# Kernel tuning notes

Hardware: AMD Instinct MI355X
Metric: run time of the kernel (lower is better)

Reference implementation:

```python
import jax, jax.numpy as jnp
import numpy as np
from jax import lax

HID = 2048; NK = 16; NV = 32; DK = 128; DV = 128; KSZ = 4; CHUNK = 64; S = 2048
KEY_DIM = NK * DK; VAL_DIM = NV * DV; CONV_DIM = 2 * KEY_DIM + VAL_DIM
EPS = 1e-6


def l2norm(x, eps=1e-6):
    return x * lax.rsqrt((x * x).sum(-1, keepdims=True) + eps)


def chunk_gated_delta_rule(q, k, v, g, beta, chunk=CHUNK):
    # q,k: [B,S,Hv,DK]; v: [B,S,Hv,DV]; g,beta: [B,S,Hv]
    q = l2norm(q); k = l2norm(k)  # use_qk_l2norm_in_kernel=True
    q, k, v = (jnp.swapaxes(x, 1, 2) for x in (q, k, v))  # [B,H,S,D]
    g = jnp.swapaxes(g, 1, 2); beta = jnp.swapaxes(beta, 1, 2)  # [B,H,S]
    B, H, Ssz, Dk = k.shape; Dv = v.shape[-1]
    N = Ssz // chunk  # seq_len chosen divisible by chunk -> pad is no-op
    q = q * (Dk ** -0.5)
    vb = v * beta[..., None]
    kb = k * beta[..., None]
    rs = lambda x: x.reshape(B, H, N, chunk, x.shape[-1])
    q, k, v, kb, vb = map(rs, (q, k, v, kb, vb))
    g = jnp.cumsum(g.reshape(B, H, N, chunk), axis=-1)
    tril = jnp.tril(jnp.ones((chunk, chunk), bool))
    stril = jnp.tril(jnp.ones((chunk, chunk), bool), -1)
    diff = jnp.where(tril, g[..., :, None] - g[..., None, :], 0.0)
    decay_mask = jnp.where(tril, jnp.exp(diff), 0.0)  # [B,H,N,C,C]
    attn = jnp.where(stril, -(kb @ jnp.swapaxes(k, -1, -2)) * decay_mask, 0.0)
    # UT (WY) transform: sequential row updates, scan over in-chunk index
    def ut_body(a, i):
        row = jnp.take(a, i, axis=-2)  # [B,H,N,C]
        new = row + jnp.einsum('bhnk,bhnkj->bhnj', row, a)
        return a.at[:, :, :, i, :].set(new), None
    attn, _ = lax.scan(ut_body, attn, jnp.arange(1, chunk))
    attn = attn + jnp.eye(chunk, dtype=attn.dtype)
    u = attn @ vb                                   # [B,H,N,C,DV]
    kcd = attn @ (kb * jnp.exp(g)[..., None])       # [B,H,N,C,DK]
    init = jnp.zeros((B, H, Dk, Dv), q.dtype)
    def step(state, inp):
        q_i, k_i, u_i, kcd_i, g_i, dm_i = inp
        scores = (q_i @ jnp.swapaxes(k_i, -1, -2)) * dm_i
        v_new = u_i - kcd_i @ state
        inter = (q_i * jnp.exp(g_i)[..., None]) @ state
        o = inter + scores @ v_new
        gl = g_i[..., -1]  # [B,H]
        state = state * jnp.exp(gl)[..., None, None] + jnp.einsum(
            'bhcd,bhce->bhde', k_i * jnp.exp(gl[..., None] - g_i)[..., None], v_new)
        return state, o
    mv = lambda x: jnp.moveaxis(x, 2, 0)
    _, out = lax.scan(step, init, (mv(q), mv(k), mv(u), mv(kcd), mv(g), mv(decay_mask)))
    out = jnp.moveaxis(out, 0, 2).reshape(B, H, Ssz, Dv)
    return jnp.swapaxes(out, 1, 2)  # [B,S,H,DV]


def setup_inputs() -> dict:
    key = jax.random.key(0)
    ks = jax.random.split(key, 8)
    return {
        'hidden_states': jax.random.normal(ks[0], (S, HID), jnp.float32),
        'W_qkv': jax.random.normal(ks[1], (CONV_DIM, HID), jnp.float32) * 0.02,
        'W_z': jax.random.normal(ks[2], (VAL_DIM, HID), jnp.float32) * 0.02,
        'W_a': jax.random.normal(ks[3], (NV, HID), jnp.float32) * 0.02,
        'W_b': jax.random.normal(ks[4], (NV, HID), jnp.float32) * 0.02,
        'conv_w': jax.random.normal(ks[5], (CONV_DIM, 1, KSZ), jnp.float32) * 0.1,
        'dt_bias': jnp.ones((NV,), jnp.float32),
        'A_log': jnp.log(jax.random.uniform(ks[6], (NV,), jnp.float32, 0.1, 16.0)),
        'norm_w': jnp.ones((DV,), jnp.float32),
        'W_out': jax.random.normal(ks[7], (HID, VAL_DIM), jnp.float32) * 0.02,
    }


def reference(hidden_states, W_qkv, W_z, W_a, W_b, conv_w, dt_bias, A_log, norm_w, W_out):
    x = hidden_states  # [S, HID]
    mixed = x @ W_qkv.T  # [S, CONV_DIM]
    z = (x @ W_z.T).reshape(-1, DV)  # [S*NV, DV]
    a = x @ W_a.T  # [S, NV]
    b = x @ W_b.T
    # causal depthwise conv1d (torch pads K-1 both sides then slices [:S])
    conv = lax.conv_general_dilated(
        mixed.T[None], conv_w, (1,), [(KSZ - 1, 0)],
        dimension_numbers=('NCH', 'OIH', 'NCH'), feature_group_count=CONV_DIM)
    mixed = jax.nn.silu(conv[0].T)  # [S, CONV_DIM]
    q = mixed[:, :KEY_DIM].reshape(1, S, NK, DK)
    k = mixed[:, KEY_DIM:2 * KEY_DIM].reshape(1, S, NK, DK)
    v = mixed[:, 2 * KEY_DIM:].reshape(1, S, NV, DV)
    beta = jax.nn.sigmoid(b)[None]  # [1,S,NV]
    g = (-jnp.exp(A_log) * jax.nn.softplus(a + dt_bias))[None]  # [1,S,NV]
    ratio = NV // NK
    q = jnp.repeat(q, ratio, axis=2)
    k = jnp.repeat(k, ratio, axis=2)
    core = chunk_gated_delta_rule(q, k, v, g, beta)  # [1,S,NV,DV]
    h = core.reshape(-1, DV)  # [S*NV, DV]
    var = jnp.mean(h * h, axis=-1, keepdims=True)
    h = h * lax.rsqrt(var + EPS) * norm_w
    h = h * jax.nn.silu(z)
    out = h.reshape(S, VAL_DIM) @ W_out.T  # [S, HID]
    return out
```

## Files before the change

### kernel.cpp

```cpp
#include <hip/hip_runtime.h>
#include <hip/hip_bf16.h>
#include <math.h>

#define S_LEN   2048
#define HIDDIM  2048
#define NKH     16
#define NVH     32
#define DKD     128
#define DVD     128
#define CCH     64
#define NCHK    32
#define KEY_DIM 2048
#define VAL_DIM 4096
#define CONV_DIM 8192

#define PA_LDS_BYTES (16384 + 16384 + 32768 + 4096 + 4096 + 256 + 256 + 256)
#define PB_LDS_BYTES ((2 * 29696 + 2048 + 1024 + 1024) * 2 + 2048 * 4)
#define G256_LDS_BYTES (3 * 16384 * 2)
#define G128_LDS_BYTES (3 * 8192 * 2)

typedef __bf16 bf16x8 __attribute__((ext_vector_type(8)));
typedef float f32x4 __attribute__((ext_vector_type(4)));

__device__ __forceinline__ float sigmoid_f(float x) { return 1.f / (1.f + __expf(-x)); }
__device__ __forceinline__ float silu_f(float x) { return x * sigmoid_f(x); }
__device__ __forceinline__ ushort f2bf(float f) {
    unsigned u = __float_as_uint(f);
    u += 0x7fffu + ((u >> 16) & 1u);
    return (ushort)(u >> 16);
}
__device__ __forceinline__ float bf2f(ushort u) {
    return __uint_as_float((unsigned)u << 16);
}

#define GLL(srcp, dstp) __builtin_amdgcn_global_load_lds( \
    (const __attribute__((address_space(1))) void*)(srcp), \
    (__attribute__((address_space(3))) void*)(dstp), 16, 0, 0)

#define NX8  (S_LEN * HIDDIM / 8)
#define NQ8  (CONV_DIM * HIDDIM / 8)
#define NZ8  (VAL_DIM * HIDDIM / 8)
#define NW8  (HIDDIM * VAL_DIM / 8)
#define NA8  (256 * HIDDIM / 8)
__global__ __launch_bounds__(256) void cast5_kernel(
    const float* __restrict__ x, const float* __restrict__ Wq,
    const float* __restrict__ Wz, const float* __restrict__ Wo,
    const float* __restrict__ Wa, const float* __restrict__ Wb,
    ushort* __restrict__ xb, ushort* __restrict__ wqz, ushort* __restrict__ wob,
    ushort* __restrict__ wab)
{
    int t = blockIdx.x * 256 + threadIdx.x;
    const float* src;
    ushort* dst;
    if (t < NX8) { src = x + (size_t)t * 8; dst = xb + (size_t)t * 8; }
    else if (t < NX8 + NQ8) {
        size_t o = (size_t)(t - NX8) * 8;
        src = Wq + o; dst = wqz + o;
    } else if (t < NX8 + NQ8 + NZ8) {
        size_t o = (size_t)(t - NX8 - NQ8) * 8;
        src = Wz + o; dst = wqz + (size_t)NQ8 * 8 + o;
    } else if (t < NX8 + NQ8 + NZ8 + NW8) {
        size_t o = (size_t)(t - NX8 - NQ8 - NZ8) * 8;
        src = Wo + o; dst = wob + o;
    } else {
        int g = t - NX8 - NQ8 - NZ8 - NW8;
        int row = g >> 8;
        int c8 = (g & 255) * 8;
        dst = wab + (size_t)g * 8;
        if (row >= 64) {
            uint4 z = {0, 0, 0, 0};
            *(uint4*)dst = z;
            return;
        }
        src = (row < 32) ? (Wa + (size_t)row * HIDDIM + c8)
                         : (Wb + (size_t)(row - 32) * HIDDIM + c8);
    }
    float4 v0 = *(const float4*)(src);
    float4 v1 = *(const float4*)(src + 4);
    union { ushort u[8]; uint4 v; } r;
    r.u[0] = f2bf(v0.x); r.u[1] = f2bf(v0.y); r.u[2] = f2bf(v0.z); r.u[3] = f2bf(v0.w);
    r.u[4] = f2bf(v1.x); r.u[5] = f2bf(v1.y); r.u[6] = f2bf(v1.z); r.u[7] = f2bf(v1.w);
    *(uint4*)dst = r.v;
}

__global__ __launch_bounds__(512, 1) void gemm256_kernel(
    const ushort* __restrict__ A, const ushort* __restrict__ B,
    ushort* __restrict__ C0, ushort* __restrict__ C1, float* __restrict__ C2,
    int K, int NS1, int NS2, int ldc0, int ldc1, int ldc2)
{
    extern __shared__ ushort g2s[];
    const int tid = threadIdx.x;
    const int wv = tid >> 6, ln = tid & 63;
    const int wm = wv >> 1, wn = wv & 1;
    const int lrow = ln & 15, lkg = ln >> 4;
    const int bid = blockIdx.y * 49 + blockIdx.x;
    const int swz = (bid & 7) * 49 + (bid >> 3);
    const int bm = (swz / 49) * 256, bn = (swz % 49) * 256;

    int soff[2];
#pragma unroll
    for (int j = 0; j < 2; ++j) {
        int g = tid + j * 512;
        int l = g & 63;
        soff[j] = (((g >> 6) * 16) + (l & 15)) * K + (l >> 4) * 8;
    }
    const ushort* Abase = A + (size_t)bm * K;
    const ushort* Bbase = B + (size_t)bn * K;

    f32x4 acc[4][8];
#pragma unroll
    for (int m = 0; m < 4; ++m)
#pragma unroll
        for (int n = 0; n < 8; ++n) {
            f32x4 z = {0.f, 0.f, 0.f, 0.f};
            acc[m][n] = z;
        }

#define G256_STAGE(bb, k0) do {                                            \
        ushort* bufA_ = g2s + (bb) * 16384;                                \
        ushort* bufB_ = bufA_ + 8192;                                      \
        _Pragma("unroll")                                                  \
        for (int j_ = 0; j_ < 2; ++j_) {                                   \
            GLL(Abase + soff[j_] + (k0), bufA_ + (j_ * 512 + wv * 64) * 8);\
            GLL(Bbase + soff[j_] + (k0), bufB_ + (j_ * 512 + wv * 64) * 8);\
        }                                                                  \
    } while (0)

    const int T = K >> 5;
    G256_STAGE(0, 0);
    G256_STAGE(1, 32);
    int bb = 0;
    for (int t = 0; t < T; ++t) {
        if (t + 1 < T) {
            asm volatile("s_waitcnt vmcnt(4)" ::: "memory");
        } else {
            asm volatile("s_waitcnt vmcnt(0)" ::: "memory");
        }
        __builtin_amdgcn_s_barrier();
        if (t + 2 < T) G256_STAGE((bb >= 1) ? (bb - 1) : (bb + 2), (t + 2) * 32);
        const ushort* LA = g2s + bb * 16384;
        const ushort* LB = LA + 8192;
        __builtin_amdgcn_s_setprio(1);
        {
            bf16x8 afv[4], bfv[8];
#pragma unroll
            for (int mf = 0; mf < 4; ++mf)
                afv[mf] = *(const bf16x8*)&LA[((wm * 4 + mf) * 64 + ln) * 8];
#pragma unroll
            for (int nf = 0; nf < 8; ++nf)
                bfv[nf] = *(const bf16x8*)&LB[((wn * 8 + nf) * 64 + ln) * 8];
#pragma unroll
            for (int mf = 0; mf < 4; ++mf)
#pragma unroll
                for (int nf = 0; nf < 8; ++nf)
                    acc[mf][nf] = __builtin_amdgcn_mfma_f32_16x16x32_bf16(
                        afv[mf], bfv[nf], acc[mf][nf], 0, 0, 0);
        }
        __builtin_amdgcn_s_setprio(0);
        bb = (bb == 2) ? 0 : bb + 1;
    }
#undef G256_STAGE

    if (bn < NS2) {
        const bool inC1 = (bn >= NS1);
        ushort* Cp = inC1 ? C1 : C0;
        const int ldc = inC1 ? ldc1 : ldc0;
        const int cboff = bn + wn * 128 - (inC1 ? NS1 : 0);
#pragma unroll
        for (int mf = 0; mf < 4; ++mf) {
            const int row0 = bm + wm * 64 + mf * 16 + lkg * 4;
#pragma unroll
            for (int nf = 0; nf < 8; ++nf) {
                ushort* cp = Cp + (size_t)row0 * ldc + cboff + nf * 16 + lrow;
#pragma unroll
                for (int j = 0; j < 4; ++j) cp[(size_t)j * ldc] = f2bf(acc[mf][nf][j]);
            }
        }
    } else {
        const int cboff = bn + wn * 128 - NS2;
#pragma unroll
        for (int mf = 0; mf < 4; ++mf) {
            const int row0 = bm + wm * 64 + mf * 16 + lkg * 4;
#pragma unroll
            for (int nf = 0; nf < 8; ++nf) {
                float* cp = C2 + (size_t)row0 * ldc2 + cboff + nf * 16 + lrow;
#pragma unroll
                for (int j = 0; j < 4; ++j) cp[(size_t)j * ldc2] = acc[mf][nf][j];
            }
        }
    }
}

__global__ __launch_bounds__(256, 2) void gemm128_kernel(
    const ushort* __restrict__ A, const ushort* __restrict__ B,
    float* __restrict__ C, int N, int K)
{
    extern __shared__ ushort g1s[];
    const int tid = threadIdx.x;
    const int wv = tid >> 6, ln = tid & 63;
    const int wm = wv >> 1, wn = wv & 1;
    const int lrow = ln & 15, lkg = ln >> 4;
    const int bm = blockIdx.y * 128, bn = blockIdx.x * 128;

    int soff[2];
#pragma unroll
    for (int j = 0; j < 2; ++j) {
        int g = tid + j * 256;
        int l = g & 63;
        soff[j] = (((g >> 6) * 16) + (l & 15)) * K + (l >> 4) * 8;
    }
    const ushort* Abase = A + (size_t)bm * K;
    const ushort* Bbase = B + (size_t)bn * K;

    f32x4 acc[4][4];
#pragma unroll
    for (int m = 0; m < 4; ++m)
#pragma unroll
        for (int n = 0; n < 4; ++n) {
            f32x4 z = {0.f, 0.f, 0.f, 0.f};
            acc[m][n] = z;
        }

#define G128_STAGE(bb, k0) do {                                            \
        ushort* bufA_ = g1s + (bb) * 8192;                                 \
        ushort* bufB_ = bufA_ + 4096;                                      \
        _Pragma("unroll")                                                  \
        for (int j_ = 0; j_ < 2; ++j_) {                                   \
            GLL(Abase + soff[j_] + (k0), bufA_ + (j_ * 256 + wv * 64) * 8);\
            GLL(Bbase + soff[j_] + (k0), bufB_ + (j_ * 256 + wv * 64) * 8);\
        }                                                                  \
    } while (0)

    const int T = K >> 5;
    G128_STAGE(0, 0);
    G128_STAGE(1, 32);
    int bb = 0;
    for (int t = 0; t < T; ++t) {
        if (t + 1 < T) {
            asm volatile("s_waitcnt vmcnt(4)" ::: "memory");
        } else {
            asm volatile("s_waitcnt vmcnt(0)" ::: "memory");
        }
        __builtin_amdgcn_s_barrier();
        if (t + 2 < T) G128_STAGE((bb >= 1) ? (bb - 1) : (bb + 2), (t + 2) * 32);
        const ushort* LA = g1s + bb * 8192;
        const ushort* LB = LA + 4096;
        __builtin_amdgcn_s_setprio(1);
        {
            bf16x8 afv[4], bfv[4];
#pragma unroll
            for (int mf = 0; mf < 4; ++mf)
                afv[mf] = *(const bf16x8*)&LA[((wm * 4 + mf) * 64 + ln) * 8];
#pragma unroll
            for (int nf = 0; nf < 4; ++nf)
                bfv[nf] = *(const bf16x8*)&LB[((wn * 4 + nf) * 64 + ln) * 8];
#pragma unroll
            for (int mf = 0; mf < 4; ++mf)
#pragma unroll
                for (int nf = 0; nf < 4; ++nf)
                    acc[mf][nf] = __builtin_amdgcn_mfma_f32_16x16x32_bf16(
                        afv[mf], bfv[nf], acc[mf][nf], 0, 0, 0);
        }
        __builtin_amdgcn_s_setprio(0);
        bb = (bb == 2) ? 0 : bb + 1;
    }
#undef G128_STAGE

#pragma unroll
    for (int mf = 0; mf < 4; ++mf) {
        const int row0 = bm + wm * 64 + mf * 16 + lkg * 4;
#pragma unroll
        for (int nf = 0; nf < 4; ++nf) {
            float* cp = C + (size_t)row0 * N + bn + wn * 64 + nf * 16 + lrow;
#pragma unroll
            for (int j = 0; j < 4; ++j) cp[(size_t)j * N] = acc[mf][nf][j];
        }
    }
}

__global__ __launch_bounds__(256) void front_kernel(
    const ushort* __restrict__ pre, const float* __restrict__ cw,
    ushort* __restrict__ qnb, ushort* __restrict__ knb, ushort* __restrict__ vbuf)
{
    __shared__ float stage[4096];
    __shared__ float sums[32];
    __shared__ float scal[32];
    const int s = blockIdx.x;
    const int tid = threadIdx.x;

#pragma unroll
    for (int cg = 0; cg < 8; ++cg) {
        const int c = cg * 1024 + tid * 4;
        float w[4][4];
#pragma unroll
        for (int j = 0; j < 4; ++j) {
            float4 wj = *(const float4*)(cw + (size_t)(c + j) * 4);
            w[j][0] = wj.x; w[j][1] = wj.y; w[j][2] = wj.z; w[j][3] = wj.w;
        }
        float a0 = 0.f, a1 = 0.f, a2 = 0.f, a3 = 0.f;
#pragma unroll
        for (int t = 0; t < 4; ++t) {
            int ss = s - 3 + t;
            if (ss >= 0) {
                uint2 xv = *(const uint2*)(pre + (size_t)ss * CONV_DIM + c);
                a0 = fmaf(bf2f((ushort)xv.x), w[0][t], a0);
                a1 = fmaf(bf2f((ushort)(xv.x >> 16)), w[1][t], a1);
                a2 = fmaf(bf2f((ushort)xv.y), w[2][t], a2);
                a3 = fmaf(bf2f((ushort)(xv.y >> 16)), w[3][t], a3);
            }
        }
        a0 = silu_f(a0); a1 = silu_f(a1); a2 = silu_f(a2); a3 = silu_f(a3);
        if (cg < 4) {
            float4 v4 = make_float4(a0, a1, a2, a3);
            *(float4*)&stage[c] = v4;
            float ss2 = a0 * a0 + a1 * a1 + a2 * a2 + a3 * a3;
#pragma unroll
            for (int m = 1; m < 32; m <<= 1) ss2 += __shfl_xor(ss2, m, 32);
            if ((tid & 31) == 0) sums[c >> 7] = ss2;
        } else {
            union { ushort u2[4]; uint2 v; } p;
            p.u2[0] = f2bf(a0); p.u2[1] = f2bf(a1);
            p.u2[2] = f2bf(a2); p.u2[3] = f2bf(a3);
            *(uint2*)(vbuf + (size_t)s * VAL_DIM + (c - 4096)) = p.v;
        }
    }
    __syncthreads();
    if (tid < 32) {
        float sc = rsqrtf(sums[tid] + 1e-6f);
        if (tid < 16) sc *= 0.08838834764831843f;
        scal[tid] = sc;
    }
    __syncthreads();
#pragma unroll
    for (int j = 0; j < 4; ++j) {
        const int c = j * 1024 + tid * 4;
        float4 v4 = *(const float4*)&stage[c];
        const float sc = scal[c >> 7];
        union { ushort u2[4]; uint2 v; } p;
        p.u2[0] = f2bf(v4.x * sc); p.u2[1] = f2bf(v4.y * sc);
        p.u2[2] = f2bf(v4.z * sc); p.u2[3] = f2bf(v4.w * sc);
        if (c < 2048)
            *(uint2*)(qnb + ((size_t)(s * NKH + (c >> 7))) * DKD + (c & 127)) = p.v;
        else
            *(uint2*)(knb + ((size_t)(s * NKH + ((c >> 7) - 16))) * DKD + (c & 127)) = p.v;
    }
}

__global__ __launch_bounds__(256) void gb_kernel(
    const float* __restrict__ ab, const float* __restrict__ dt_bias,
    const float* __restrict__ A_log, float* __restrict__ g, float* __restrict__ beta)
{
    int idx = blockIdx.x * 256 + threadIdx.x;
    int s = idx >> 5, h = idx & 31;
    float av = ab[(size_t)s * 256 + h] + dt_bias[h];
    float sp = (av > 20.f) ? av : log1pf(__expf(av));
    g[idx] = -__expf(A_log[h]) * sp;
    beta[idx] = sigmoid_f(ab[(size_t)s * 256 + 32 + h]);
}

__global__ __launch_bounds__(256) void phaseA_kernel(
    const ushort* __restrict__ qnb, const ushort* __restrict__ knb,
    const ushort* __restrict__ vbuf, const float* __restrict__ gbuf,
    const float* __restrict__ betabuf,
    ushort* __restrict__ u, ushort* __restrict__ kcd,
    ushort* __restrict__ scores, float* __restrict__ gcs_out,
    ushort* __restrict__ knT)
{
    extern __shared__ char pasm[];
    ushort* kb    = (ushort*)(pasm);
    ushort* qb    = (ushort*)(pasm + 16384);
    ushort* Xb    = (ushort*)(pasm + 32768);
    float*  Adiag = (float*)(pasm + 65536);
    ushort* Ab    = (ushort*)(pasm + 69632);
    float*  gcs_s = (float*)(pasm + 73728);
    float*  bet_s = (float*)(pasm + 73984);
    float*  scK_s = (float*)(pasm + 74240);
    float*  Pf    = (float*)qb;

    const int n = blockIdx.x, h = blockIdx.y, kh = h >> 1;
    const int tid = threadIdx.x;
    const int s0 = n * CCH;
    const int wv = tid >> 6, ln = tid & 63;
    const int lrow = ln & 15, lkg = ln >> 4;

    float xr[64];
    if (tid < 128) {
        const ushort* vp = vbuf + (size_t)s0 * VAL_DIM + h * DVD + tid;
#pragma unroll
        for (int i = 0; i < 64; ++i) xr[i] = bf2f(vp[(size_t)i * VAL_DIM]);
    } else {
        const ushort* kp = knb + ((size_t)s0 * NKH + kh) * DKD + (tid - 128);
#pragma unroll
        for (int i = 0; i < 64; ++i) xr[i] = bf2f(kp[(size_t)i * (NKH * DKD)]);
    }

    {
        uint4 z = {0, 0, 0, 0};
#pragma unroll
        for (int i = 0; i < 8; ++i)
            *(uint4*)&Xb[(i * 256 + tid) * 8] = z;
        *(uint4*)&Ab[tid * 8] = z;
    }

    if (tid < 64) {
        float gv = gbuf[(size_t)(s0 + tid) * NVH + h];
#pragma unroll
        for (int off = 1; off < 64; off <<= 1) {
            float pv = __shfl_up(gv, off, 64);
            if (tid >= off) gv += pv;
        }
        float bv = betabuf[(size_t)(s0 + tid) * NVH + h];
        gcs_s[tid] = gv;
        bet_s[tid] = bv;
        scK_s[tid] = bv * __expf(gv);
        gcs_out[(size_t)h * S_LEN + s0 + tid] = gv;
    }

    {
        const int r = tid >> 2, c0 = (tid & 3) * 32;
        const int mbase = (((r >> 4) * 4 + (tid & 3)) * 64 + (r & 15)) * 8;
        const ushort* ksrc = knb + ((size_t)(s0 + r) * NKH + kh) * DKD + c0;
        const ushort* qsrc = qnb + ((size_t)(s0 + r) * NKH + kh) * DKD + c0;
#pragma unroll
        for (int j0 = 0; j0 < 4; ++j0) {
            *(uint4*)&kb[mbase + (j0 << 7)] = *(const uint4*)(ksrc + j0 * 8);
            *(uint4*)&qb[mbase + (j0 << 7)] = *(const uint4*)(qsrc + j0 * 8);
        }
    }
    __syncthreads();

    f32x4 accA[4], accQ[4];
#pragma unroll
    for (int j = 0; j < 4; ++j) {
        f32x4 z = {0.f, 0.f, 0.f, 0.f};
        accA[j] = z; accQ[j] = z;
    }
#pragma unroll
    for (int ks = 0; ks < 4; ++ks) {
        bf16x8 a_k = *(const bf16x8*)&kb[((wv * 4 + ks) * 64 + ln) * 8];
        bf16x8 a_q = *(const bf16x8*)&qb[((wv * 4 + ks) * 64 + ln) * 8];
#pragma unroll
        for (int j = 0; j < 4; ++j) {
            bf16x8 b_k = *(const bf16x8*)&kb[((j * 4 + ks) * 64 + ln) * 8];
            accA[j] = __builtin_amdgcn_mfma_f32_16x16x32_bf16(a_k, b_k, accA[j], 0, 0, 0);
            accQ[j] = __builtin_amdgcn_mfma_f32_16x16x32_bf16(a_q, b_k, accQ[j], 0, 0, 0);
        }
    }
    {
        ushort* scp = scores + (size_t)(h * NCHK + n) * (CCH * CCH);
#pragma unroll
        for (int j = 0; j < 4; ++j) {
            const int c = j * 16 + lrow;
            const float gc = gcs_s[c];
#pragma unroll
            for (int jj = 0; jj < 4; ++jj) {
                const int i = wv * 16 + lkg * 4 + jj;
                const float e = __expf(gcs_s[i] - gc);
                float sv = (i >= c) ? (accQ[j][jj] * e) : 0.f;
                scp[i * CCH + c] = f2bf(sv);
                float aval = (i > c) ? (-bet_s[i] * accA[j][jj] * e) : 0.f;
                if (j == wv) {
                    Adiag[wv * 256 + (i & 15) * 16 + lrow] = aval;
                } else if (j < wv) {
                    const int f = (wv == 1) ? 0 : ((wv == 2) ? 1 : (2 + (j >> 1)));
                    const int lk = ((j & 1) << 4) | lrow;
                    const int lane2 = (i & 15) | ((lk >> 3) << 4);
                    Ab[(f * 64 + lane2) * 8 + (lk & 7)] = f2bf(aval);
                }
            }
        }
    }
    if (tid < 128) {
#pragma unroll
        for (int i4 = 0; i4 < 16; ++i4) {
            float4 b4 = *(const float4*)&bet_s[i4 * 4];
            xr[i4 * 4 + 0] *= b4.x; xr[i4 * 4 + 1] *= b4.y;
            xr[i4 * 4 + 2] *= b4.z; xr[i4 * 4 + 3] *= b4.w;
        }
    } else {
#pragma unroll
        for (int i4 = 0; i4 < 16; ++i4) {
            float4 b4 = *(const float4*)&scK_s[i4 * 4];
            xr[i4 * 4 + 0] *= b4.x; xr[i4 * 4 + 1] *= b4.y;
            xr[i4 * 4 + 2] *= b4.z; xr[i4 * 4 + 3] *= b4.w;
        }
    }
    __syncthreads();

    const int ct = tid >> 4, lct = tid & 15;
#pragma unroll
    for (int s = 0; s < 4; ++s) {
        float y[16];
        float pr[16];
        if (s > 0) {
#pragma unroll
            for (int r = 0; r < 16; ++r) pr[r] = Pf[r * 256 + tid];
        } else {
#pragma unroll
            for (int r = 0; r < 16; ++r) pr[r] = 0.f;
        }
#pragma unroll
        for (int r = 0; r < 16; ++r) {
            float acc = xr[s * 16 + r] + pr[r];
#pragma unroll
            for (int k4 = 0; k4 < 16; k4 += 4) {
                if (k4 < r) {
                    float4 a4 = *(const float4*)&Adiag[s * 256 + r * 16 + k4];
                    if (k4 + 0 < r) acc = fmaf(a4.x, y[k4 + 0], acc);
                    if (k4 + 1 < r) acc = fmaf(a4.y, y[k4 + 1], acc);
                    if (k4 + 2 < r) acc = fmaf(a4.z, y[k4 + 2], acc);
                    if (k4 + 3 < r) acc = fmaf(a4.w, y[k4 + 3], acc);
                }
            }
            y[r] = acc;
        }
        if (tid < 128) {
            ushort* up = u + (size_t)(h * NCHK + n) * (CCH * DVD) + (s * 16) * DVD + tid;
#pragma unroll
            for (int r = 0; r < 16; ++r) up[r * DVD] = f2bf(y[r]);
        } else {
            ushort* kp = kcd + (size_t)(h * NCHK + n) * (CCH * DKD) + (s * 16) * DKD + (tid - 128);
#pragma unroll
            for (int r = 0; r < 16; ++r) kp[r * DKD] = f2bf(y[r]);
        }
        if (s < 3) {
#pragma unroll
            for (int half = 0; half < 2; ++half) {
                union { ushort us[8]; uint4 v; } p;
#pragma unroll
                for (int e = 0; e < 8; ++e) p.us[e] = f2bf(y[half * 8 + e]);
                const int kg = (s & 1) * 2 + half;
                *(uint4*)&Xb[(((s >> 1) * 16 + ct) * 64 + (kg * 16 + lct)) * 8] = p.v;
            }
            __syncthreads();
            const int snx = s + 1;
            const int nT2 = (snx + 1) >> 1;
            f32x4 accP[4];
#pragma unroll
            for (int ctl = 0; ctl < 4; ++ctl) {
                f32x4 z = {0.f, 0.f, 0.f, 0.f};
                accP[ctl] = z;
            }
#pragma unroll
            for (int t2 = 0; t2 < 2; ++t2) {
                if (t2 < nT2) {
                    const int f = (snx == 1) ? 0 : ((snx == 2) ? 1 : (2 + t2));
                    bf16x8 a = *(const bf16x8*)&Ab[(f * 64 + ln) * 8];
#pragma unroll
                    for (int ctl = 0; ctl < 4; ++ctl) {
                        bf16x8 b = *(const bf16x8*)&Xb[((t2 * 16 + wv * 4 + ctl) * 64 + ln) * 8];
                        accP[ctl] = __builtin_amdgcn_mfma_f32_16x16x32_bf16(a, b, accP[ctl], 0, 0, 0);
                    }
                }
            }
#pragma unroll
            for (int ctl = 0; ctl < 4; ++ctl)
#pragma unroll
                for (int jj = 0; jj < 4; ++jj)
                    Pf[(lkg * 4 + jj) * 256 + wv * 64 + ctl * 16 + lrow] = accP[ctl][jj];
            __syncthreads();
        }
    }

    if (!(h & 1)) {
        const int dk = tid >> 1, ch = (tid & 1) * 32;
        ushort* dst = knT + ((size_t)(kh * NCHK + n) * DKD + dk) * CCH + ch;
        const int kpart = ((dk >> 5) * 64) * 8 + (((dk >> 3) & 3) << 4) * 8 + (dk & 7);
#pragma unroll
        for (int j0 = 0; j0 < 32; j0 += 8) {
            union { ushort us[8]; uint4 v; } p;
#pragma unroll
            for (int j = 0; j < 8; ++j) {
                const int row = ch + j0 + j;
                p.us[j] = kb[((row >> 4) * 4 * 64 + (row & 15)) * 8 + kpart];
            }
            *(uint4*)(dst + j0) = p.v;
        }
    }
}

__global__ __launch_bounds__(256) void phaseB_kernel(
    const ushort* __restrict__ qnb, const ushort* __restrict__ knT,
    const ushort* __restrict__ u, const ushort* __restrict__ kcd,
    const ushort* __restrict__ sc, const float* __restrict__ gcs,
    ushort* __restrict__ obuf)
{
    extern __shared__ ushort smu[];
    ushort* storg  = smu + 59392;
    ushort* vnorg  = smu + 61440;
    ushort* vnsorg = smu + 62464;
    float*  gcsall = (float*)(smu + 63488);

    const int h = blockIdx.x;
    const int dvb = blockIdx.y;
    const int d0 = dvb * 16;
    const int kh = h >> 1;
    const int tid = threadIdx.x;
    const int wv = tid >> 6, ln = tid & 63;
    const int lrow = ln & 15, lkg = ln >> 4;

    {
        uint4 z = {0, 0, 0, 0};
        *(uint4*)&storg[tid * 8] = z;
    }

    const int q_lane  = lrow * (NKH * DKD) + kh * DKD + wv * 32 + lkg * 8;
    const int kc_lane = lrow * DKD + wv * 32 + lkg * 8;
    const int st_lane = ((tid >> 7) * 16 + lrow) * 64 + ((tid >> 6) & 1) * 32 + lkg * 8;
    const int dst_e   = wv * 512;

#define PBSTG(bsel, nn) do {                                                  \
        const ushort* qsrc_  = qnb + (size_t)((nn) * CCH) * (NKH * DKD);      \
        const ushort* kcsrc_ = kcd + (size_t)(h * NCHK + (nn)) * (CCH * DKD); \
        const ushort* scsrc_ = sc  + (size_t)(h * NCHK + (nn)) * (CCH * CCH); \
        const ushort* kTsrc_ = knT + (size_t)(kh * NCHK + (nn)) * (DKD * CCH);\
        const ushort* usrc_  = u   + (size_t)(h * NCHK + (nn)) * (CCH * DVD) + d0; \
        ushort* base_ = smu + (bsel) * 29696;                                 \
        _Pragma("unroll")                                                     \
        for (int r_ = 0; r_ < 4; ++r_) {                                      \
            GLL(qsrc_ + q_lane + r_ * 32768, base_ + r_ * 2048 + dst_e);      \
            GLL(kcsrc_ + kc_lane + r_ * 2048, base_ + 8192 + r_ * 2048 + dst_e); \
            GLL(kTsrc_ + st_lane + r_ * 2048, base_ + 20480 + r_ * 2048 + dst_e); \
        }                                                                     \
        _Pragma("unroll")                                                     \
        for (int r_ = 0; r_ < 2; ++r_)                                        \
            GLL(scsrc_ + st_lane + r_ * 2048, base_ + 16384 + r_ * 2048 + dst_e); \
        if (tid < 128)                                                        \
            GLL(usrc_ + (tid >> 1) * DVD + (tid & 1) * 8, base_ + 28672 + tid * 8); \
    } while (0)

    PBSTG(0, 0);
    {
        float4 g0 = *(const float4*)(gcs + (size_t)h * S_LEN + tid * 8);
        float4 g1 = *(const float4*)(gcs + (size_t)h * S_LEN + tid * 8 + 4);
        *(float4*)&gcsall[tid * 8] = g0;
        *(float4*)&gcsall[tid * 8 + 4] = g1;
    }
    __syncthreads();

    f32x4 accS0 = {0.f, 0.f, 0.f, 0.f}, accS1 = {0.f, 0.f, 0.f, 0.f};

    for (int n = 0; n < NCHK; ++n) {
        const int cur = n & 1;
        if (n + 1 < NCHK) PBSTG(cur ^ 1, n + 1);
        const ushort* qorg  = smu + cur * 29696;
        const ushort* kcorg = qorg + 8192;
        const ushort* scorg = qorg + 16384;
        const ushort* kTorg = qorg + 20480;
        const ushort* uorg  = qorg + 28672;
        const float*  gcs_s = gcsall + n * 64;
        const int s0 = n * CCH;

        f32x4 accv = {0.f, 0.f, 0.f, 0.f};
        f32x4 acco = {0.f, 0.f, 0.f, 0.f};
#pragma unroll
        for (int ks = 0; ks < 4; ++ks) {
            bf16x8 b_st = *(const bf16x8*)&storg[(ks * 64 + ln) * 8];
            bf16x8 a_kc = *(const bf16x8*)&kcorg[((wv * 4 + ks) * 64 + ln) * 8];
            bf16x8 a_q  = *(const bf16x8*)&qorg[((wv * 4 + ks) * 64 + ln) * 8];
            accv = __builtin_amdgcn_mfma_f32_16x16x32_bf16(a_kc, b_st, accv, 0, 0, 0);
            acco = __builtin_amdgcn_mfma_f32_16x16x32_bf16(a_q, b_st, acco, 0, 0, 0);
        }
        const int row = wv * 16 + lkg * 4;
        float u0 = bf2f(uorg[(row + 0) * 16 + lrow]);
        float u1 = bf2f(uorg[(row + 1) * 16 + lrow]);
        float u2 = bf2f(uorg[(row + 2) * 16 + lrow]);
        float u3 = bf2f(uorg[(row + 3) * 16 + lrow]);
        const float gl = gcs_s[63];
        float vn0 = u0 - accv[0], vn1 = u1 - accv[1];
        float vn2 = u2 - accv[2], vn3 = u3 - accv[3];
        {
            float g0 = gcs_s[row], g1 = gcs_s[row + 1], g2 = gcs_s[row + 2], g3 = gcs_s[row + 3];
            acco[0] *= __expf(g0); acco[1] *= __expf(g1);
            acco[2] *= __expf(g2); acco[3] *= __expf(g3);
            const int eb = ((wv >> 1) * 64 + ((wv & 1) * 2 + (lkg >> 1)) * 16 + lrow) * 8
                         + (lkg & 1) * 4;
            union { ushort u2a[4]; uint2 v; } pa, pb;
            pa.u2a[0] = f2bf(vn0); pa.u2a[1] = f2bf(vn1);
            pa.u2a[2] = f2bf(vn2); pa.u2a[3] = f2bf(vn3);
            pb.u2a[0] = f2bf(vn0 * __expf(gl - g0)); pb.u2a[1] = f2bf(vn1 * __expf(gl - g1));
            pb.u2a[2] = f2bf(vn2 * __expf(gl - g2)); pb.u2a[3] = f2bf(vn3 * __expf(gl - g3));
            *(uint2*)&vnorg[eb] = pa.v;
            *(uint2*)&vnsorg[eb] = pb.v;
        }
        __syncthreads();

#pragma unroll
        for (int ks = 0; ks < 2; ++ks) {
            bf16x8 a_sc = *(const bf16x8*)&scorg[((wv * 2 + ks) * 64 + ln) * 8];
            bf16x8 b_vn = *(const bf16x8*)&vnorg[(ks * 64 + ln) * 8];
            acco = __builtin_amdgcn_mfma_f32_16x16x32_bf16(a_sc, b_vn, acco, 0, 0, 0);
        }
        ushort* op = obuf + (size_t)(s0 + row) * VAL_DIM + h * DVD + d0 + lrow;
        op[0] = f2bf(acco[0]); op[VAL_DIM] = f2bf(acco[1]);
        op[2 * VAL_DIM] = f2bf(acco[2]); op[3 * VAL_DIM] = f2bf(acco[3]);

        const float egl = __expf(gl);
        accS0 *= egl; accS1 *= egl;
#pragma unroll
        for (int ks = 0; ks < 2; ++ks) {
            bf16x8 a_vs = *(const bf16x8*)&vnsorg[(ks * 64 + ln) * 8];
            bf16x8 b_k0 = *(const bf16x8*)&kTorg[(((wv * 2 + 0) * 2 + ks) * 64 + ln) * 8];
            bf16x8 b_k1 = *(const bf16x8*)&kTorg[(((wv * 2 + 1) * 2 + ks) * 64 + ln) * 8];
            accS0 = __builtin_amdgcn_mfma_f32_16x16x32_bf16(a_vs, b_k0, accS0, 0, 0, 0);
            accS1 = __builtin_amdgcn_mfma_f32_16x16x32_bf16(a_vs, b_k1, accS1, 0, 0, 0);
        }
#pragma unroll
        for (int j = 0; j < 4; ++j) {
            storg[(wv * 64 + ((lrow >> 3)) * 16 + lkg * 4 + j) * 8 + (lrow & 7)] = f2bf(accS0[j]);
            storg[(wv * 64 + (2 + (lrow >> 3)) * 16 + lkg * 4 + j) * 8 + (lrow & 7)] = f2bf(accS1[j]);
        }
        __syncthreads();
    }
#undef PBSTG
}

__global__ __launch_bounds__(256) void norm_kernel(
    const ushort* __restrict__ obuf, const ushort* __restrict__ z,
    const float* __restrict__ nw, ushort* __restrict__ hbuf)
{
    int row = (blockIdx.x * 256 + threadIdx.x) >> 6;
    int lane = threadIdx.x & 63;
    uint ov = *(const uint*)(obuf + (size_t)row * DVD + lane * 2);
    float x0 = bf2f((ushort)ov), x1 = bf2f((ushort)(ov >> 16));
    float ss = x0 * x0 + x1 * x1;
#pragma unroll
    for (int m = 1; m < 64; m <<= 1) ss += __shfl_xor(ss, m, 64);
    float scale = rsqrtf(ss * (1.f / DVD) + 1e-6f);
    uint zv = *(const uint*)(z + (size_t)row * DVD + lane * 2);
    float z0 = bf2f((ushort)zv), z1 = bf2f((ushort)(zv >> 16));
    float2 w2 = *(const float2*)(nw + lane * 2);
    float h0 = x0 * scale * w2.x * silu_f(z0);
    float h1 = x1 * scale * w2.y * silu_f(z1);
    union { ushort u[2]; uint v; } r;
    r.u[0] = f2bf(h0); r.u[1] = f2bf(h1);
    *(uint*)(hbuf + (size_t)row * DVD + lane * 2) = r.v;
}

extern "C" void kernel_launch(void* const* d_in, const int* in_sizes, int n_in,
                              void* d_out, int out_size, void* d_ws, size_t ws_size,
                              hipStream_t stream)
{
    (void)in_sizes; (void)n_in; (void)out_size; (void)ws_size;
    const float* x      = (const float*)d_in[0];
    const float* W_qkv  = (const float*)d_in[1];
    const float* W_z    = (const float*)d_in[2];
    const float* W_a    = (const float*)d_in[3];
    const float* W_b    = (const float*)d_in[4];
    const float* conv_w = (const float*)d_in[5];
    const float* dt_b   = (const float*)d_in[6];
    const float* A_log  = (const float*)d_in[7];
    const float* norm_w = (const float*)d_in[8];
    const float* W_out  = (const float*)d_in[9];
    float* out = (float*)d_out;

    char* ws = (char*)d_ws;
    ushort* mixed_pre = (ushort*)(ws);
    ushort* u_buf     = (ushort*)(ws);
    ushort* kcd_buf   = (ushort*)(ws + 33554432);
    ushort* knT_buf   = (ushort*)(ws + 50331648);
    ushort* wqz       = (ushort*)(ws + 67108864);
    ushort* wab       = (ushort*)(ws + 117440512);
    ushort* xb        = (ushort*)(ws + 118489088);
    ushort* vbuf      = (ushort*)(ws + 67108864);
    ushort* obuf      = (ushort*)(ws + 83886080);
    ushort* hbuf      = (ushort*)(ws + 100663296);
    ushort* z_buf     = (ushort*)(ws + 134217728);
    ushort* sc_buf    = (ushort*)(ws + 167772160);
    float*  ab_buf    = (float*)(ws + 167772160);
    ushort* qnb       = (ushort*)(ws + 176160768);
    ushort* knb       = (ushort*)(ws + 184549376);
    float*  g_buf     = (float*)(ws + 201326592);
    float*  bet_buf   = (float*)(ws + 201588736);
    float*  gcs_buf   = (float*)(ws + 201850880);
    ushort* wob       = (ushort*)(ws + 202113024);

    hipFuncSetAttribute((const void*)phaseA_kernel,
                        hipFuncAttributeMaxDynamicSharedMemorySize, PA_LDS_BYTES);
    hipFuncSetAttribute((const void*)phaseB_kernel,
                        hipFuncAttributeMaxDynamicSharedMemorySize, PB_LDS_BYTES);
    hipFuncSetAttribute((const void*)gemm256_kernel,
                        hipFuncAttributeMaxDynamicSharedMemorySize, G256_LDS_BYTES);
    hipFuncSetAttribute((const void*)gemm128_kernel,
                        hipFuncAttributeMaxDynamicSharedMemorySize, G128_LDS_BYTES);

    dim3 blk(256);
    cast5_kernel<<<(NX8 + NQ8 + NZ8 + NW8 + NA8) / 256, blk, 0, stream>>>(
        x, W_qkv, W_z, W_out, W_a, W_b, xb, wqz, wob, wab);
    gemm256_kernel<<<dim3(49, S_LEN / 256), dim3(512), G256_LDS_BYTES, stream>>>(
        xb, wqz, mixed_pre, z_buf, ab_buf, HIDDIM,
        CONV_DIM, CONV_DIM + VAL_DIM, CONV_DIM, VAL_DIM, 256);
    front_kernel<<<S_LEN, blk, 0, stream>>>(mixed_pre, conv_w, qnb, knb, vbuf);
    gb_kernel<<<(S_LEN * NVH) / 256, blk, 0, stream>>>(ab_buf, dt_b, A_log, g_buf, bet_buf);
    phaseA_kernel<<<dim3(NCHK, NVH), blk, PA_LDS_BYTES, stream>>>(
        qnb, knb, vbuf, g_buf, bet_buf, u_buf, kcd_buf, sc_buf, gcs_buf, knT_buf);
    phaseB_kernel<<<dim3(NVH, 8), blk, PB_LDS_BYTES, stream>>>(
        qnb, knT_buf, u_buf, kcd_buf, sc_buf, gcs_buf, obuf);
    norm_kernel<<<(S_LEN * NVH * 64) / 256, blk, 0, stream>>>(obuf, z_buf, norm_w, hbuf);
    gemm128_kernel<<<dim3(HIDDIM / 128, S_LEN / 128), blk, G128_LDS_BYTES, stream>>>(
        hbuf, wob, out, HIDDIM, VAL_DIM);
}
```

Measured before the change: 408.5 us.

## Load GEMM A operand directly to registers and fuse gate computation into phaseA

In the large input-projection GEMM, the A tile is no longer staged through LDS. Each lane reads its A fragments straight from global memory into registers, which halves the LDS footprint and cuts the async copies per stage. The loop now issues its fragment loads before prefetching the next stage and places the barrier after the MFMAs. Separately, the small g/beta kernel is removed and its softplus/sigmoid math moves into phaseA's prologue, which saves a launch and an intermediate buffer. The risk is that uncached, strided direct global loads of A may stall the MFMA pipeline more than LDS staging did.

```diff
diff --git a/kernel.cpp b/kernel.cpp
--- a/kernel.cpp
+++ b/kernel.cpp
@@ -16,7 +16,7 @@
 
 #define PA_LDS_BYTES (16384 + 16384 + 32768 + 4096 + 4096 + 256 + 256 + 256)
 #define PB_LDS_BYTES ((2 * 29696 + 2048 + 1024 + 1024) * 2 + 2048 * 4)
-#define G256_LDS_BYTES (3 * 16384 * 2)
+#define G256_LDS_BYTES (3 * 8192 * 2)
 #define G128_LDS_BYTES (3 * 8192 * 2)
 
 typedef __bf16 bf16x8 __attribute__((ext_vector_type(8)));
@@ -104,8 +104,8 @@
         int l = g & 63;
         soff[j] = (((g >> 6) * 16) + (l & 15)) * K + (l >> 4) * 8;
     }
-    const ushort* Abase = A + (size_t)bm * K;
     const ushort* Bbase = B + (size_t)bn * K;
+    const ushort* Alane = A + (size_t)(bm + wm * 64 + lrow) * K + lkg * 8;
 
     f32x4 acc[4][8];
 #pragma unroll
@@ -117,46 +117,43 @@
         }
 
 #define G256_STAGE(bb, k0) do {                                            \
-        ushort* bufA_ = g2s + (bb) * 16384;                                \
-        ushort* bufB_ = bufA_ + 8192;                                      \
+        ushort* bufB_ = g2s + (bb) * 8192;                                 \
         _Pragma("unroll")                                                  \
-        for (int j_ = 0; j_ < 2; ++j_) {                                   \
-            GLL(Abase + soff[j_] + (k0), bufA_ + (j_ * 512 + wv * 64) * 8);\
+        for (int j_ = 0; j_ < 2; ++j_)                                     \
             GLL(Bbase + soff[j_] + (k0), bufB_ + (j_ * 512 + wv * 64) * 8);\
-        }                                                                  \
     } while (0)
 
     const int T = K >> 5;
     G256_STAGE(0, 0);
     G256_STAGE(1, 32);
+    asm volatile("s_waitcnt vmcnt(2)" ::: "memory");
+    __builtin_amdgcn_s_barrier();
     int bb = 0;
     for (int t = 0; t < T; ++t) {
-        if (t + 1 < T) {
-            asm volatile("s_waitcnt vmcnt(4)" ::: "memory");
+        const ushort* LB = g2s + bb * 8192;
+        bf16x8 bfv[8];
+#pragma unroll
+        for (int nf = 0; nf < 8; ++nf)
+            bfv[nf] = *(const bf16x8*)&LB[((wn * 8 + nf) * 64 + ln) * 8];
+        bf16x8 afv[4];
+#pragma unroll
+        for (int mf = 0; mf < 4; ++mf)
+            afv[mf] = *(const bf16x8*)(Alane + (size_t)(mf * 16) * K + t * 32);
+        if (t + 2 < T) G256_STAGE((bb >= 1) ? (bb - 1) : (bb + 2), (t + 2) * 32);
+        if (t + 2 < T) {
+            asm volatile("s_waitcnt vmcnt(2)" ::: "memory");
         } else {
             asm volatile("s_waitcnt vmcnt(0)" ::: "memory");
         }
+        __builtin_amdgcn_s_setprio(1);
+#pragma unroll
+        for (int mf = 0; mf < 4; ++mf)
+#pragma unroll
+            for (int nf = 0; nf < 8; ++nf)
+                acc[mf][nf] = __builtin_amdgcn_mfma_f32_16x16x32_bf16(
+                    afv[mf], bfv[nf], acc[mf][nf], 0, 0, 0);
+        __builtin_amdgcn_s_setprio(0);
         __builtin_amdgcn_s_barrier();
-        if (t + 2 < T) G256_STAGE((bb >= 1) ? (bb - 1) : (bb + 2), (t + 2) * 32);
-        const ushort* LA = g2s + bb * 16384;
-        const ushort* LB = LA + 8192;
-        __builtin_amdgcn_s_setprio(1);
-        {
-            bf16x8 afv[4], bfv[8];
-#pragma unroll
-            for (int mf = 0; mf < 4; ++mf)
-                afv[mf] = *(const bf16x8*)&LA[((wm * 4 + mf) * 64 + ln) * 8];
-#pragma unroll
-            for (int nf = 0; nf < 8; ++nf)
-                bfv[nf] = *(const bf16x8*)&LB[((wn * 8 + nf) * 64 + ln) * 8];
-#pragma unroll
-            for (int mf = 0; mf < 4; ++mf)
-#pragma unroll
-                for (int nf = 0; nf < 8; ++nf)
-                    acc[mf][nf] = __builtin_amdgcn_mfma_f32_16x16x32_bf16(
-                        afv[mf], bfv[nf], acc[mf][nf], 0, 0, 0);
-        }
-        __builtin_amdgcn_s_setprio(0);
         bb = (bb == 2) ? 0 : bb + 1;
     }
 #undef G256_STAGE
@@ -346,22 +343,10 @@
     }
 }
 
-__global__ __launch_bounds__(256) void gb_kernel(
-    const float* __restrict__ ab, const float* __restrict__ dt_bias,
-    const float* __restrict__ A_log, float* __restrict__ g, float* __restrict__ beta)
-{
-    int idx = blockIdx.x * 256 + threadIdx.x;
-    int s = idx >> 5, h = idx & 31;
-    float av = ab[(size_t)s * 256 + h] + dt_bias[h];
-    float sp = (av > 20.f) ? av : log1pf(__expf(av));
-    g[idx] = -__expf(A_log[h]) * sp;
-    beta[idx] = sigmoid_f(ab[(size_t)s * 256 + 32 + h]);
-}
-
 __global__ __launch_bounds__(256) void phaseA_kernel(
     const ushort* __restrict__ qnb, const ushort* __restrict__ knb,
-    const ushort* __restrict__ vbuf, const float* __restrict__ gbuf,
-    const float* __restrict__ betabuf,
+    const ushort* __restrict__ vbuf, const float* __restrict__ ab,
+    const float* __restrict__ dt_bias, const float* __restrict__ A_log,
     ushort* __restrict__ u, ushort* __restrict__ kcd,
     ushort* __restrict__ scores, float* __restrict__ gcs_out,
     ushort* __restrict__ knT)
@@ -403,13 +388,15 @@
     }
 
     if (tid < 64) {
-        float gv = gbuf[(size_t)(s0 + tid) * NVH + h];
+        float av = ab[(size_t)(s0 + tid) * 256 + h] + dt_bias[h];
+        float sp = (av > 20.f) ? av : log1pf(__expf(av));
+        float gv = -__expf(A_log[h]) * sp;
 #pragma unroll
         for (int off = 1; off < 64; off <<= 1) {
             float pv = __shfl_up(gv, off, 64);
             if (tid >= off) gv += pv;
         }
-        float bv = betabuf[(size_t)(s0 + tid) * NVH + h];
+        float bv = sigmoid_f(ab[(size_t)(s0 + tid) * 256 + 32 + h]);
         gcs_s[tid] = gv;
         bet_s[tid] = bv;
         scK_s[tid] = bv * __expf(gv);
@@ -767,11 +754,9 @@
     ushort* hbuf      = (ushort*)(ws + 100663296);
     ushort* z_buf     = (ushort*)(ws + 134217728);
     ushort* sc_buf    = (ushort*)(ws + 167772160);
-    float*  ab_buf    = (float*)(ws + 167772160);
     ushort* qnb       = (ushort*)(ws + 176160768);
     ushort* knb       = (ushort*)(ws + 184549376);
-    float*  g_buf     = (float*)(ws + 201326592);
-    float*  bet_buf   = (float*)(ws + 201588736);
+    float*  ab_buf    = (float*)(ws + 192937984);
     float*  gcs_buf   = (float*)(ws + 201850880);
     ushort* wob       = (ushort*)(ws + 202113024);
 
@@ -791,9 +776,8 @@
         xb, wqz, mixed_pre, z_buf, ab_buf, HIDDIM,
         CONV_DIM, CONV_DIM + VAL_DIM, CONV_DIM, VAL_DIM, 256);
     front_kernel<<<S_LEN, blk, 0, stream>>>(mixed_pre, conv_w, qnb, knb, vbuf);
-    gb_kernel<<<(S_LEN * NVH) / 256, blk, 0, stream>>>(ab_buf, dt_b, A_log, g_buf, bet_buf);
     phaseA_kernel<<<dim3(NCHK, NVH), blk, PA_LDS_BYTES, stream>>>(
-        qnb, knb, vbuf, g_buf, bet_buf, u_buf, kcd_buf, sc_buf, gcs_buf, knT_buf);
+        qnb, knb, vbuf, ab_buf, dt_b, A_log, u_buf, kcd_buf, sc_buf, gcs_buf, knT_buf);
     phaseB_kernel<<<dim3(NVH, 8), blk, PB_LDS_BYTES, stream>>>(
         qnb, knT_buf, u_buf, kcd_buf, sc_buf, gcs_buf, obuf);
     norm_kernel<<<(S_LEN * NVH * 64) / 256, blk, 0, stream>>>(obuf, z_buf, norm_w, hbuf);
```

Measured after the change: 515.6 us. 26.2% more time.
